# Optimization experiments

Measured on AMD Instinct MI355X. Metric: run time of the kernel, lower is better.

## Reference

```python
import jax, jax.numpy as jnp
import numpy as np

# Kernel offset table copied VERBATIM from the source (note the duplicated
# [-1,-1] row where [-1,1] would be expected -- we replicate the bug).
OFF = jnp.array([[-1, -1], [-1, 0], [-1, -1], [0, -1], [0, 0], [0, 1],
                 [1, -1], [1, 0], [1, 1]], dtype=jnp.float32)  # (9, 2)

T_HARD = 3.14 / 6
S_HARD = 2.0
S_RANGE = (S_HARD - 1.0 / S_HARD) / 2.0
H_VEC = jnp.array([T_HARD, S_RANGE, S_RANGE], dtype=jnp.float32)
B_VEC = jnp.array([0.0, S_RANGE, S_RANGE], dtype=jnp.float32)
BN_EPS = 1e-5


def setup_inputs() -> dict:
    key = jax.random.key(0)
    ks = jax.random.split(key, 9)
    N, C, H, W, O = 8, 128, 64, 64, 128
    return {
        "input_feat": jax.random.normal(ks[0], (N, C, H, W), jnp.float32),
        "ste_w": 0.05 * jax.random.normal(ks[1], (3, C, 1, 1), jnp.float32),
        "ste_b": 0.05 * jax.random.normal(ks[2], (3,), jnp.float32),
        "bn_gamma": 1.0 + 0.1 * jax.random.normal(ks[3], (3,), jnp.float32),
        "bn_beta": 0.1 * jax.random.normal(ks[4], (3,), jnp.float32),
        "bn_mean": 0.1 * jax.random.normal(ks[5], (3,), jnp.float32),
        "bn_var": jax.random.uniform(ks[6], (3,), jnp.float32, 0.5, 1.5),
        "dconv_w": jax.random.normal(ks[7], (O, C, 3, 3), jnp.float32) / np.sqrt(C * 9.0),
        "dconv_b": 0.05 * jax.random.normal(ks[8], (O,), jnp.float32),
    }


def _forward(input_feat, ste_w, ste_b, bn_gamma, bn_beta, bn_mean, bn_var,
             dconv_w, dconv_b):
    N, C, H, W = input_feat.shape
    O = dconv_w.shape[0]
    # --- ste: 1x1 conv -> BatchNorm (eval) -> tanh, then affine H*x + B ---
    s = jnp.einsum('nchw,oc->nohw', input_feat, ste_w[:, :, 0, 0])
    s = s + ste_b[None, :, None, None]
    scale = (bn_gamma / jnp.sqrt(bn_var + BN_EPS))
    s = (s - bn_mean[None, :, None, None]) * scale[None, :, None, None] \
        + bn_beta[None, :, None, None]
    info = jnp.tanh(s) * H_VEC[None, :, None, None] + B_VEC[None, :, None, None]
    # --- per-pixel 2x2 scaled rotation applied to kernel grid ---
    theta = info[:, 0]                  # [N,H,W]
    sin = jnp.sin(theta)
    cos = jnp.cos(theta)
    a00 = cos * info[:, 1]
    a11 = cos * info[:, 2]
    awt = jnp.stack([a00, -sin, sin, a11], axis=-1).reshape(N, H, W, 2, 2)
    offs = jnp.einsum('kd,nhwde->nkhwe', OFF, awt)   # [N,9,H,W,2]
    off_y = offs[..., 0]
    off_x = offs[..., 1]
    # --- deformable 3x3 conv, stride 1, padding 1, zero-pad bilinear ---
    k = jnp.arange(9)
    dy = (k // 3 - 1).astype(jnp.float32)  # default kernel y-offsets
    dx = (k % 3 - 1).astype(jnp.float32)
    yy = jnp.arange(H, dtype=jnp.float32)
    xx = jnp.arange(W, dtype=jnp.float32)
    y = yy[None, None, :, None] + dy[None, :, None, None] + off_y  # [N,9,H,W]
    x = xx[None, None, None, :] + dx[None, :, None, None] + off_x
    y0 = jnp.floor(y)
    x0 = jnp.floor(x)
    wy = y - y0
    wx = x - x0
    y0i = y0.astype(jnp.int32)
    x0i = x0.astype(jnp.int32)

    def gather(img, yi, xi):
        # img [C,H,W], yi/xi [9,H,W] -> [C,9,H,W], zero outside bounds
        valid = (yi >= 0) & (yi < H) & (xi >= 0) & (xi < W)
        v = img[:, jnp.clip(yi, 0, H - 1), jnp.clip(xi, 0, W - 1)]
        return v * valid[None].astype(img.dtype)

    def sample_one(img, y0i, x0i, wy, wx):
        v00 = gather(img, y0i, x0i)
        v01 = gather(img, y0i, x0i + 1)
        v10 = gather(img, y0i + 1, x0i)
        v11 = gather(img, y0i + 1, x0i + 1)
        return (v00 * ((1 - wy) * (1 - wx))[None]
                + v01 * ((1 - wy) * wx)[None]
                + v10 * (wy * (1 - wx))[None]
                + v11 * (wy * wx)[None])

    samp = jax.vmap(sample_one)(input_feat, y0i, x0i, wy, wx)  # [N,C,9,H,W]
    out = jnp.einsum('nckhw,ock->nohw', samp, dconv_w.reshape(O, C, 9))
    return out + dconv_b[None, :, None, None]


def reference(input_feat, ste_w, ste_b, bn_gamma, bn_beta, bn_mean, bn_var,
              dconv_w, dconv_b):
    return _forward(input_feat, ste_w, ste_b, bn_gamma, bn_beta, bn_mean,
                    bn_var, dconv_w, dconv_b)
```

## Files before the change

### kernel.cpp

```cpp
#include <hip/hip_runtime.h>

constexpr int kN = 8, kC = 128, kH = 64, kW = 64, kO = 128;
constexpr int kHW = kH * kW;

typedef float f32x4 __attribute__((ext_vector_type(4)));
typedef short bf16x8 __attribute__((ext_vector_type(8)));
typedef unsigned short ushort8 __attribute__((ext_vector_type(8)));

__device__ __forceinline__ float bf2f(unsigned short u) {
  unsigned int x = ((unsigned int)u) << 16;
  return __builtin_bit_cast(float, x);
}
__device__ __forceinline__ unsigned short f2bf(float f) {
  unsigned int b = __builtin_bit_cast(unsigned int, f);
  b += 0x7FFFu + ((b >> 16) & 1u);
  return (unsigned short)(b >> 16);
}

__global__ __launch_bounds__(256) void prep_kernel(
    const float* __restrict__ inp, const float* __restrict__ ste_w,
    const float* __restrict__ ste_b, const float* __restrict__ bn_g,
    const float* __restrict__ bn_b, const float* __restrict__ bn_m,
    const float* __restrict__ bn_v, unsigned short* __restrict__ nhwc,
    float* __restrict__ prm) {
  __shared__ float tile[kC * kW];
  __shared__ float part[4][3][kW];
  const int tid = threadIdx.x;
  const int nh = blockIdx.x;
  const int n = nh >> 6, h = nh & 63;
  const float* base = inp + (size_t)n * kC * kHW + h * kW;

  for (int i = tid; i < kC * kW; i += 256) {
    int c = i >> 6, w = i & 63;
    tile[i] = base[c * kHW + w];
  }
  __syncthreads();

  {
    const int w = tid & 63, cg = tid >> 6;
    float s0 = 0.f, s1 = 0.f, s2 = 0.f;
#pragma unroll 8
    for (int j = 0; j < 32; ++j) {
      int c = cg * 32 + j;
      float v = tile[c * kW + w];
      s0 += v * ste_w[c];
      s1 += v * ste_w[kC + c];
      s2 += v * ste_w[2 * kC + c];
    }
    part[cg][0][w] = s0;
    part[cg][1][w] = s1;
    part[cg][2][w] = s2;
  }
  __syncthreads();
  if (tid < kW) {
    const int w = tid;
    float s0 = part[0][0][w] + part[1][0][w] + part[2][0][w] + part[3][0][w];
    float s1 = part[0][1][w] + part[1][1][w] + part[2][1][w] + part[3][1][w];
    float s2 = part[0][2][w] + part[1][2][w] + part[2][2][w] + part[3][2][w];
    s0 = (s0 + ste_b[0] - bn_m[0]) * (bn_g[0] * rsqrtf(bn_v[0] + 1e-5f)) + bn_b[0];
    s1 = (s1 + ste_b[1] - bn_m[1]) * (bn_g[1] * rsqrtf(bn_v[1] + 1e-5f)) + bn_b[1];
    s2 = (s2 + ste_b[2] - bn_m[2]) * (bn_g[2] * rsqrtf(bn_v[2] + 1e-5f)) + bn_b[2];
    float th = tanhf(s0) * (3.14f / 6.0f);
    float i1 = tanhf(s1) * 0.75f + 0.75f;
    float i2 = tanhf(s2) * 0.75f + 0.75f;
    float sn = sinf(th), cs = cosf(th);
    prm[nh * 192 + w * 3 + 0] = cs * i1;
    prm[nh * 192 + w * 3 + 1] = sn;
    prm[nh * 192 + w * 3 + 2] = cs * i2;
  }

  for (int i = tid; i < kW * 16; i += 256) {
    int w = i & 63, ch = i >> 6;
    int c0 = ch * 8;
    ushort8 v;
#pragma unroll
    for (int j = 0; j < 8; ++j) v[j] = f2bf(tile[(c0 + j) * kW + w]);
    *(ushort8*)&nhwc[((size_t)(n * kH + h) * kW + w) * kC + c0] = v;
  }
}

__global__ __launch_bounds__(256) void reorder_bf16_kernel(
    const float* __restrict__ dw, unsigned short* __restrict__ wkb) {
  int idx = blockIdx.x * blockDim.x + threadIdx.x;
  if (idx >= 9 * kO * kC) return;
  int k = idx / (kO * kC);
  int r = idx - k * (kO * kC);
  int o = r >> 7, c = r & 127;
  wkb[idx] = f2bf(dw[(o * kC + c) * 9 + k]);
}

__global__ __launch_bounds__(512) void deform_mfma_kernel(
    const unsigned short* __restrict__ nhwc,
    const unsigned short* __restrict__ wkb,
    const float* __restrict__ prm, const float* __restrict__ db,
    float* __restrict__ out) {
  __shared__ __align__(16) unsigned short As[32 * 128];
  __shared__ __align__(16) unsigned short Bs[128 * 128];
  __shared__ float prmS[32 * 3];

  const int tid = threadIdx.x;
  const int lane = tid & 63, wave = tid >> 6;
  const int nh = blockIdx.x >> 1;
  const int w0 = (blockIdx.x & 1) << 5;
  const int n = nh >> 6, h = nh & 63;
  const unsigned short* nhwc_n = nhwc + (size_t)n * kH * kW * kC;

  if (tid < 96) prmS[tid] = prm[nh * 192 + w0 * 3 + tid];

  const int mg = wave >> 2, ng = wave & 3;
  const int row = mg * 16 + (lane & 15);
  const int kq = lane >> 4;
  const int rsw = (row & 7) << 4;
  f32x4 acc[2];
  acc[0] = (f32x4){0.f, 0.f, 0.f, 0.f};
  acc[1] = (f32x4){0.f, 0.f, 0.f, 0.f};

  for (int k = 0; k < 9; ++k) {
    __syncthreads();
    const float fdy = (float)(k / 3 - 1);
    const float fdx = (float)(k % 3 - 1);
    const float o0 = fdy;
    const float o1 = (k == 2) ? -1.0f : fdx;

    const unsigned short* wkp = wkb + (size_t)k * kO * kC;
#pragma unroll
    for (int it = 0; it < 4; ++it) {
      int i = tid + it * 512;
      int o = i >> 4, ch = i & 15;
      ushort8 v = *(const ushort8*)&wkp[o * kC + ch * 8];
      *(ushort8*)((char*)Bs + o * 256 + ((ch * 16) ^ ((o & 7) << 4))) = v;
    }

    {
      int p = tid >> 4, ch = tid & 15;
      float a00 = prmS[p * 3], sn = prmS[p * 3 + 1], a11 = prmS[p * 3 + 2];
      float y = (float)h + fdy + o0 * a00 + o1 * sn;
      float x = (float)(w0 + p) + fdx - o0 * sn + o1 * a11;
      float y0f = floorf(y), x0f = floorf(x);
      float wy = y - y0f, wx = x - x0f;
      int y0 = (int)y0f, x0 = (int)x0f;
      bool yv0 = (unsigned)y0 < (unsigned)kH;
      bool yv1 = (unsigned)(y0 + 1) < (unsigned)kH;
      bool xv0 = (unsigned)x0 < (unsigned)kW;
      bool xv1 = (unsigned)(x0 + 1) < (unsigned)kW;
      int y0c = min(max(y0, 0), kH - 1);
      int y1c = min(max(y0 + 1, 0), kH - 1);
      int x0c = min(max(x0, 0), kW - 1);
      int x1c = min(max(x0 + 1, 0), kW - 1);
      float w00 = (1.f - wy) * (1.f - wx) * (yv0 && xv0 ? 1.f : 0.f);
      float w01 = (1.f - wy) * wx * (yv0 && xv1 ? 1.f : 0.f);
      float w10 = wy * (1.f - wx) * (yv1 && xv0 ? 1.f : 0.f);
      float w11 = wy * wx * (yv1 && xv1 ? 1.f : 0.f);
      const int cb = ch * 8;
      ushort8 v00 = *(const ushort8*)&nhwc_n[((y0c * kW) + x0c) * kC + cb];
      ushort8 v01 = *(const ushort8*)&nhwc_n[((y0c * kW) + x1c) * kC + cb];
      ushort8 v10 = *(const ushort8*)&nhwc_n[((y1c * kW) + x0c) * kC + cb];
      ushort8 v11 = *(const ushort8*)&nhwc_n[((y1c * kW) + x1c) * kC + cb];
      ushort8 r;
#pragma unroll
      for (int j = 0; j < 8; ++j) {
        float val = bf2f(v00[j]) * w00 + bf2f(v01[j]) * w01 +
                    bf2f(v10[j]) * w10 + bf2f(v11[j]) * w11;
        r[j] = f2bf(val);
      }
      *(ushort8*)((char*)As + p * 256 + ((ch * 16) ^ ((p & 7) << 4))) = r;
    }
    __syncthreads();

#pragma unroll
    for (int ks = 0; ks < 4; ++ks) {
      const int kb = ks * 64 + kq * 16;
      bf16x8 a = *(const bf16x8*)((char*)As + row * 256 + (kb ^ rsw));
#pragma unroll
      for (int f = 0; f < 2; ++f) {
        const int orow = (ng * 2 + f) * 16 + (lane & 15);
        bf16x8 b = *(const bf16x8*)((char*)Bs + orow * 256 +
                                    (kb ^ ((orow & 7) << 4)));
        acc[f] = __builtin_amdgcn_mfma_f32_16x16x32_bf16(a, b, acc[f], 0, 0, 0);
      }
    }
  }

  const int pixb = mg * 16 + (lane >> 4) * 4;
#pragma unroll
  for (int f = 0; f < 2; ++f) {
    const int o = (ng * 2 + f) * 16 + (lane & 15);
    const float bias = db[o];
    float4 v = {acc[f][0] + bias, acc[f][1] + bias, acc[f][2] + bias,
                acc[f][3] + bias};
    *(float4*)&out[((size_t)(n * kO + o)) * kHW + h * kW + w0 + pixb] = v;
  }
}

__global__ __launch_bounds__(256) void deform_kernel_f32(
    const float* __restrict__ inp, const float* __restrict__ ste_w,
    const float* __restrict__ ste_b, const float* __restrict__ bn_g,
    const float* __restrict__ bn_b, const float* __restrict__ bn_m,
    const float* __restrict__ bn_v, const float* __restrict__ dw,
    const float* __restrict__ db, float* __restrict__ out) {
  __shared__ __align__(16) float smp[kC * 16];
  __shared__ float prm[16][3];
  const int tid = threadIdx.x;
  const int base = blockIdx.x * 16;
  const int n = base / kHW;
  const int hw = base - n * kHW;
  const int h = hw / kW;
  const int w0 = hw - h * kW;
  const float* inp_n = inp + (size_t)n * kC * kHW;

  for (int i = tid; i < kC * 16; i += 256) {
    int c = i >> 4, p = i & 15;
    smp[i] = inp_n[c * kHW + h * kW + w0 + p];
  }
  __syncthreads();
  {
    const int p = tid >> 4, cl = tid & 15;
    float a0 = 0.f, a1 = 0.f, a2 = 0.f;
#pragma unroll
    for (int i = 0; i < 8; ++i) {
      int c = cl + (i << 4);
      float v = smp[c * 16 + p];
      a0 += v * ste_w[c];
      a1 += v * ste_w[kC + c];
      a2 += v * ste_w[2 * kC + c];
    }
#pragma unroll
    for (int off = 8; off; off >>= 1) {
      a0 += __shfl_down(a0, off, 16);
      a1 += __shfl_down(a1, off, 16);
      a2 += __shfl_down(a2, off, 16);
    }
    if (cl == 0) {
      float s0 = (a0 + ste_b[0] - bn_m[0]) * (bn_g[0] * rsqrtf(bn_v[0] + 1e-5f)) + bn_b[0];
      float s1 = (a1 + ste_b[1] - bn_m[1]) * (bn_g[1] * rsqrtf(bn_v[1] + 1e-5f)) + bn_b[1];
      float s2 = (a2 + ste_b[2] - bn_m[2]) * (bn_g[2] * rsqrtf(bn_v[2] + 1e-5f)) + bn_b[2];
      float th = tanhf(s0) * (3.14f / 6.0f);
      float i1 = tanhf(s1) * 0.75f + 0.75f;
      float i2 = tanhf(s2) * 0.75f + 0.75f;
      prm[p][0] = cosf(th) * i1;
      prm[p][1] = sinf(th);
      prm[p][2] = cosf(th) * i2;
    }
  }
  const int o = tid & 127;
  const int ph = tid >> 7;
  float acc[8] = {0.f};
  for (int k = 0; k < 9; ++k) {
    __syncthreads();
    const float fdy = (float)(k / 3 - 1);
    const float fdx = (float)(k % 3 - 1);
    const float o0 = fdy;
    const float o1 = (k == 2) ? -1.0f : fdx;
    for (int i = tid; i < kC * 16; i += 256) {
      int c = i >> 4, p = i & 15;
      float a00 = prm[p][0], sn = prm[p][1], a11 = prm[p][2];
      float y = (float)h + fdy + o0 * a00 + o1 * sn;
      float x = (float)(w0 + p) + fdx - o0 * sn + o1 * a11;
      float y0f = floorf(y), x0f = floorf(x);
      float wy = y - y0f, wx = x - x0f;
      int y0 = (int)y0f, x0 = (int)x0f;
      const float* ic = inp_n + c * kHW;
      bool yv0 = (unsigned)y0 < (unsigned)kH;
      bool yv1 = (unsigned)(y0 + 1) < (unsigned)kH;
      bool xv0 = (unsigned)x0 < (unsigned)kW;
      bool xv1 = (unsigned)(x0 + 1) < (unsigned)kW;
      int y0c = min(max(y0, 0), kH - 1);
      int y1c = min(max(y0 + 1, 0), kH - 1);
      int x0c = min(max(x0, 0), kW - 1);
      int x1c = min(max(x0 + 1, 0), kW - 1);
      float v00 = (yv0 && xv0) ? ic[y0c * kW + x0c] : 0.f;
      float v01 = (yv0 && xv1) ? ic[y0c * kW + x1c] : 0.f;
      float v10 = (yv1 && xv0) ? ic[y1c * kW + x0c] : 0.f;
      float v11 = (yv1 && xv1) ? ic[y1c * kW + x1c] : 0.f;
      smp[i] = v00 * (1.f - wy) * (1.f - wx) + v01 * (1.f - wy) * wx +
               v10 * wy * (1.f - wx) + v11 * wy * wx;
    }
    __syncthreads();
    const float* wp = dw + (size_t)o * kC * 9 + k;
#pragma unroll 4
    for (int c = 0; c < kC; ++c) {
      float wv = wp[(size_t)c * 9];
      const float4 s0 = *(const float4*)&smp[c * 16 + (ph << 3)];
      const float4 s1 = *(const float4*)&smp[c * 16 + (ph << 3) + 4];
      acc[0] += wv * s0.x; acc[1] += wv * s0.y; acc[2] += wv * s0.z; acc[3] += wv * s0.w;
      acc[4] += wv * s1.x; acc[5] += wv * s1.y; acc[6] += wv * s1.z; acc[7] += wv * s1.w;
    }
  }
  const float bias = db[o];
  float* op = out + ((size_t)(n * kO + o)) * kHW + h * kW + w0 + (ph << 3);
#pragma unroll
  for (int j = 0; j < 8; ++j) op[j] = acc[j] + bias;
}

extern "C" void kernel_launch(void* const* d_in, const int* in_sizes, int n_in,
                              void* d_out, int out_size, void* d_ws, size_t ws_size,
                              hipStream_t stream) {
  const float* inp   = (const float*)d_in[0];
  const float* ste_w = (const float*)d_in[1];
  const float* ste_b = (const float*)d_in[2];
  const float* bn_g  = (const float*)d_in[3];
  const float* bn_b  = (const float*)d_in[4];
  const float* bn_m  = (const float*)d_in[5];
  const float* bn_v  = (const float*)d_in[6];
  const float* dw    = (const float*)d_in[7];
  const float* db    = (const float*)d_in[8];
  float* out = (float*)d_out;

  const size_t nhwc_bytes = (size_t)kN * kH * kW * kC * 2;
  const size_t wkb_bytes = (size_t)9 * kO * kC * 2;
  const size_t prm_bytes = (size_t)kN * kH * kW * 3 * 4;
  const size_t need = nhwc_bytes + wkb_bytes + prm_bytes;

  if (ws_size >= need) {
    unsigned short* nhwc = (unsigned short*)d_ws;
    unsigned short* wkb = (unsigned short*)((char*)d_ws + nhwc_bytes);
    float* prm = (float*)((char*)d_ws + nhwc_bytes + wkb_bytes);
    prep_kernel<<<kN * kH, 256, 0, stream>>>(inp, ste_w, ste_b, bn_g, bn_b,
                                             bn_m, bn_v, nhwc, prm);
    int wtot = 9 * kO * kC;
    reorder_bf16_kernel<<<(wtot + 255) / 256, 256, 0, stream>>>(dw, wkb);
    deform_mfma_kernel<<<kN * kH * 2, 512, 0, stream>>>(nhwc, wkb, prm, db, out);
  } else {
    deform_kernel_f32<<<kN * kHW / 16, 256, 0, stream>>>(
        inp, ste_w, ste_b, bn_g, bn_b, bn_m, bn_v, dw, db, out);
  }
}
```

Baseline: 53.79 us.

## Double-buffer LDS tiles and prefetch next tap's loads into registers

Each tap's weight tile and bilinear gather loads are now issued into registers before the current tap's MFMA loop, then written to the alternate LDS buffer afterward. This cuts one barrier per tap and hides global-load latency behind the matrix math. The per-pixel parameters are also loaded straight into registers instead of being staged through LDS. In exchange, LDS use roughly doubles to about 73 KB per block, which can reduce how many blocks fit per CU. The launch-bounds hint asking for 4 blocks may not be met and can raise register pressure.

```diff
diff --git a/kernel.cpp b/kernel.cpp
--- a/kernel.cpp
+++ b/kernel.cpp
@@ -89,14 +89,13 @@
   wkb[idx] = f2bf(dw[(o * kC + c) * 9 + k]);
 }
 
-__global__ __launch_bounds__(512) void deform_mfma_kernel(
+__global__ __launch_bounds__(512, 4) void deform_mfma_kernel(
     const unsigned short* __restrict__ nhwc,
     const unsigned short* __restrict__ wkb,
     const float* __restrict__ prm, const float* __restrict__ db,
     float* __restrict__ out) {
-  __shared__ __align__(16) unsigned short As[32 * 128];
-  __shared__ __align__(16) unsigned short Bs[128 * 128];
-  __shared__ float prmS[32 * 3];
+  __shared__ __align__(16) unsigned short As[2][32 * 128];
+  __shared__ __align__(16) unsigned short Bs[2][128 * 128];
 
   const int tid = threadIdx.x;
   const int lane = tid & 63, wave = tid >> 6;
@@ -105,7 +104,10 @@
   const int n = nh >> 6, h = nh & 63;
   const unsigned short* nhwc_n = nhwc + (size_t)n * kH * kW * kC;
 
-  if (tid < 96) prmS[tid] = prm[nh * 192 + w0 * 3 + tid];
+  const int p = tid >> 4, ch = tid & 15;
+  const float a00 = prm[nh * 192 + (w0 + p) * 3 + 0];
+  const float sn  = prm[nh * 192 + (w0 + p) * 3 + 1];
+  const float a11 = prm[nh * 192 + (w0 + p) * 3 + 2];
 
   const int mg = wave >> 2, ng = wave & 3;
   const int row = mg * 16 + (lane & 15);
@@ -115,70 +117,88 @@
   acc[0] = (f32x4){0.f, 0.f, 0.f, 0.f};
   acc[1] = (f32x4){0.f, 0.f, 0.f, 0.f};
 
-  for (int k = 0; k < 9; ++k) {
-    __syncthreads();
+  ushort8 bReg[4];
+  ushort8 a00r, a01r, a10r, a11r;
+  float w00, w01, w10, w11;
+
+  auto issue_tap = [&](int k) {
+    const unsigned short* wkp = wkb + (size_t)k * kO * kC;
+#pragma unroll
+    for (int it = 0; it < 4; ++it) {
+      int i = tid + it * 512;
+      int o = i >> 4, c8 = i & 15;
+      bReg[it] = *(const ushort8*)&wkp[o * kC + c8 * 8];
+    }
     const float fdy = (float)(k / 3 - 1);
     const float fdx = (float)(k % 3 - 1);
     const float o0 = fdy;
     const float o1 = (k == 2) ? -1.0f : fdx;
-
-    const unsigned short* wkp = wkb + (size_t)k * kO * kC;
+    float y = (float)h + fdy + o0 * a00 + o1 * sn;
+    float x = (float)(w0 + p) + fdx - o0 * sn + o1 * a11;
+    float y0f = floorf(y), x0f = floorf(x);
+    float wy = y - y0f, wx = x - x0f;
+    int y0 = (int)y0f, x0 = (int)x0f;
+    bool yv0 = (unsigned)y0 < (unsigned)kH;
+    bool yv1 = (unsigned)(y0 + 1) < (unsigned)kH;
+    bool xv0 = (unsigned)x0 < (unsigned)kW;
+    bool xv1 = (unsigned)(x0 + 1) < (unsigned)kW;
+    int y0c = min(max(y0, 0), kH - 1);
+    int y1c = min(max(y0 + 1, 0), kH - 1);
+    int x0c = min(max(x0, 0), kW - 1);
+    int x1c = min(max(x0 + 1, 0), kW - 1);
+    w00 = (1.f - wy) * (1.f - wx) * (yv0 && xv0 ? 1.f : 0.f);
+    w01 = (1.f - wy) * wx * (yv0 && xv1 ? 1.f : 0.f);
+    w10 = wy * (1.f - wx) * (yv1 && xv0 ? 1.f : 0.f);
+    w11 = wy * wx * (yv1 && xv1 ? 1.f : 0.f);
+    const int cb = ch * 8;
+    a00r = *(const ushort8*)&nhwc_n[((y0c * kW) + x0c) * kC + cb];
+    a01r = *(const ushort8*)&nhwc_n[((y0c * kW) + x1c) * kC + cb];
+    a10r = *(const ushort8*)&nhwc_n[((y1c * kW) + x0c) * kC + cb];
+    a11r = *(const ushort8*)&nhwc_n[((y1c * kW) + x1c) * kC + cb];
+  };
+
+  auto write_tiles = [&](int buf) {
 #pragma unroll
     for (int it = 0; it < 4; ++it) {
       int i = tid + it * 512;
-      int o = i >> 4, ch = i & 15;
-      ushort8 v = *(const ushort8*)&wkp[o * kC + ch * 8];
-      *(ushort8*)((char*)Bs + o * 256 + ((ch * 16) ^ ((o & 7) << 4))) = v;
-    }
-
-    {
-      int p = tid >> 4, ch = tid & 15;
-      float a00 = prmS[p * 3], sn = prmS[p * 3 + 1], a11 = prmS[p * 3 + 2];
-      float y = (float)h + fdy + o0 * a00 + o1 * sn;
-      float x = (float)(w0 + p) + fdx - o0 * sn + o1 * a11;
-      float y0f = floorf(y), x0f = floorf(x);
-      float wy = y - y0f, wx = x - x0f;
-      int y0 = (int)y0f, x0 = (int)x0f;
-      bool yv0 = (unsigned)y0 < (unsigned)kH;
-      bool yv1 = (unsigned)(y0 + 1) < (unsigned)kH;
-      bool xv0 = (unsigned)x0 < (unsigned)kW;
-      bool xv1 = (unsigned)(x0 + 1) < (unsigned)kW;
-      int y0c = min(max(y0, 0), kH - 1);
-      int y1c = min(max(y0 + 1, 0), kH - 1);
-      int x0c = min(max(x0, 0), kW - 1);
-      int x1c = min(max(x0 + 1, 0), kW - 1);
-      float w00 = (1.f - wy) * (1.f - wx) * (yv0 && xv0 ? 1.f : 0.f);
-      float w01 = (1.f - wy) * wx * (yv0 && xv1 ? 1.f : 0.f);
-      float w10 = wy * (1.f - wx) * (yv1 && xv0 ? 1.f : 0.f);
-      float w11 = wy * wx * (yv1 && xv1 ? 1.f : 0.f);
-      const int cb = ch * 8;
-      ushort8 v00 = *(const ushort8*)&nhwc_n[((y0c * kW) + x0c) * kC + cb];
-      ushort8 v01 = *(const ushort8*)&nhwc_n[((y0c * kW) + x1c) * kC + cb];
-      ushort8 v10 = *(const ushort8*)&nhwc_n[((y1c * kW) + x0c) * kC + cb];
-      ushort8 v11 = *(const ushort8*)&nhwc_n[((y1c * kW) + x1c) * kC + cb];
-      ushort8 r;
-#pragma unroll
-      for (int j = 0; j < 8; ++j) {
-        float val = bf2f(v00[j]) * w00 + bf2f(v01[j]) * w01 +
-                    bf2f(v10[j]) * w10 + bf2f(v11[j]) * w11;
-        r[j] = f2bf(val);
-      }
-      *(ushort8*)((char*)As + p * 256 + ((ch * 16) ^ ((p & 7) << 4))) = r;
-    }
-    __syncthreads();
-
+      int o = i >> 4, c8 = i & 15;
+      *(ushort8*)((char*)Bs[buf] + o * 256 + ((c8 * 16) ^ ((o & 7) << 4))) =
+          bReg[it];
+    }
+    ushort8 r;
+#pragma unroll
+    for (int j = 0; j < 8; ++j) {
+      float val = bf2f(a00r[j]) * w00 + bf2f(a01r[j]) * w01 +
+                  bf2f(a10r[j]) * w10 + bf2f(a11r[j]) * w11;
+      r[j] = f2bf(val);
+    }
+    *(ushort8*)((char*)As[buf] + p * 256 + ((ch * 16) ^ ((p & 7) << 4))) = r;
+  };
+
+  issue_tap(0);
+  write_tiles(0);
+  __syncthreads();
+
+  for (int k = 0; k < 9; ++k) {
+    const int cur = k & 1;
+    if (k < 8) issue_tap(k + 1);
+
+    const char* Ab = (const char*)As[cur];
+    const char* Bb = (const char*)Bs[cur];
 #pragma unroll
     for (int ks = 0; ks < 4; ++ks) {
       const int kb = ks * 64 + kq * 16;
-      bf16x8 a = *(const bf16x8*)((char*)As + row * 256 + (kb ^ rsw));
+      bf16x8 a = *(const bf16x8*)(Ab + row * 256 + (kb ^ rsw));
 #pragma unroll
       for (int f = 0; f < 2; ++f) {
         const int orow = (ng * 2 + f) * 16 + (lane & 15);
-        bf16x8 b = *(const bf16x8*)((char*)Bs + orow * 256 +
-                                    (kb ^ ((orow & 7) << 4)));
+        bf16x8 b = *(const bf16x8*)(Bb + orow * 256 + (kb ^ ((orow & 7) << 4)));
         acc[f] = __builtin_amdgcn_mfma_f32_16x16x32_bf16(a, b, acc[f], 0, 0, 0);
       }
     }
+
+    if (k < 8) write_tiles(cur ^ 1);
+    __syncthreads();
   }
 
   const int pixb = mg * 16 + (lane >> 4) * 4;
```

New measurement: 51.65 us. 4.0% less time.

## Gather all nine taps into LDS once and stream weights from global memory

Applied to the files above, without the earlier changes.

The weight-reorder kernel is folded into the prep kernel as extra blocks, which removes one launch. The MFMA kernel now samples all nine kernel taps into a single padded LDS A-tile, with a stride chosen to avoid bank conflicts, and needs only one barrier. Per-tap LDS staging of the B weights is dropped: B fragments are loaded straight from global memory, relying on L2/L1 caching. Loads of the bilinear-sampling parameters also go straight from global memory. This removes 18 barriers and the B-tile copy, but B reads now hit global memory inside the MFMA loop, and the A tile is larger, which may affect occupancy.

```diff
diff --git a/kernel.cpp b/kernel.cpp
--- a/kernel.cpp
+++ b/kernel.cpp
@@ -22,11 +22,24 @@
     const float* __restrict__ ste_b, const float* __restrict__ bn_g,
     const float* __restrict__ bn_b, const float* __restrict__ bn_m,
     const float* __restrict__ bn_v, unsigned short* __restrict__ nhwc,
-    float* __restrict__ prm) {
+    float* __restrict__ prm, const float* __restrict__ dw,
+    unsigned short* __restrict__ wkb) {
+  const int bid = blockIdx.x;
+  if (bid >= kN * kH) {
+    int idx = (bid - kN * kH) * 256 + threadIdx.x;
+    if (idx < 9 * kO * kC) {
+      int k = idx / (kO * kC);
+      int r = idx - k * (kO * kC);
+      int o = r >> 7, c = r & 127;
+      wkb[idx] = f2bf(dw[(o * kC + c) * 9 + k]);
+    }
+    return;
+  }
+
   __shared__ float tile[kC * kW];
   __shared__ float part[4][3][kW];
   const int tid = threadIdx.x;
-  const int nh = blockIdx.x;
+  const int nh = bid;
   const int n = nh >> 6, h = nh & 63;
   const float* base = inp + (size_t)n * kC * kHW + h * kW;
 
@@ -79,24 +92,14 @@
   }
 }
 
-__global__ __launch_bounds__(256) void reorder_bf16_kernel(
-    const float* __restrict__ dw, unsigned short* __restrict__ wkb) {
-  int idx = blockIdx.x * blockDim.x + threadIdx.x;
-  if (idx >= 9 * kO * kC) return;
-  int k = idx / (kO * kC);
-  int r = idx - k * (kO * kC);
-  int o = r >> 7, c = r & 127;
-  wkb[idx] = f2bf(dw[(o * kC + c) * 9 + k]);
-}
-
-__global__ __launch_bounds__(512) void deform_mfma_kernel(
+constexpr int kAStride = 1160;
+
+__global__ __launch_bounds__(512, 4) void deform_mfma_kernel(
     const unsigned short* __restrict__ nhwc,
     const unsigned short* __restrict__ wkb,
     const float* __restrict__ prm, const float* __restrict__ db,
     float* __restrict__ out) {
-  __shared__ __align__(16) unsigned short As[32 * 128];
-  __shared__ __align__(16) unsigned short Bs[128 * 128];
-  __shared__ float prmS[32 * 3];
+  __shared__ __align__(16) unsigned short As[32][kAStride];
 
   const int tid = threadIdx.x;
   const int lane = tid & 63, wave = tid >> 6;
@@ -105,79 +108,72 @@
   const int n = nh >> 6, h = nh & 63;
   const unsigned short* nhwc_n = nhwc + (size_t)n * kH * kW * kC;
 
-  if (tid < 96) prmS[tid] = prm[nh * 192 + w0 * 3 + tid];
-
-  const int mg = wave >> 2, ng = wave & 3;
-  const int row = mg * 16 + (lane & 15);
-  const int kq = lane >> 4;
-  const int rsw = (row & 7) << 4;
-  f32x4 acc[2];
-  acc[0] = (f32x4){0.f, 0.f, 0.f, 0.f};
-  acc[1] = (f32x4){0.f, 0.f, 0.f, 0.f};
-
+  const int p = tid >> 4, ch = tid & 15;
+  const float a00 = prm[nh * 192 + (w0 + p) * 3 + 0];
+  const float sn  = prm[nh * 192 + (w0 + p) * 3 + 1];
+  const float a11 = prm[nh * 192 + (w0 + p) * 3 + 2];
+  const int cb = ch * 8;
+
+#pragma unroll
   for (int k = 0; k < 9; ++k) {
-    __syncthreads();
     const float fdy = (float)(k / 3 - 1);
     const float fdx = (float)(k % 3 - 1);
     const float o0 = fdy;
     const float o1 = (k == 2) ? -1.0f : fdx;
-
-    const unsigned short* wkp = wkb + (size_t)k * kO * kC;
-#pragma unroll
-    for (int it = 0; it < 4; ++it) {
-      int i = tid + it * 512;
-      int o = i >> 4, ch = i & 15;
-      ushort8 v = *(const ushort8*)&wkp[o * kC + ch * 8];
-      *(ushort8*)((char*)Bs + o * 256 + ((ch * 16) ^ ((o & 7) << 4))) = v;
-    }
-
-    {
-      int p = tid >> 4, ch = tid & 15;
-      float a00 = prmS[p * 3], sn = prmS[p * 3 + 1], a11 = prmS[p * 3 + 2];
-      float y = (float)h + fdy + o0 * a00 + o1 * sn;
-      float x = (float)(w0 + p) + fdx - o0 * sn + o1 * a11;
-      float y0f = floorf(y), x0f = floorf(x);
-      float wy = y - y0f, wx = x - x0f;
-      int y0 = (int)y0f, x0 = (int)x0f;
-      bool yv0 = (unsigned)y0 < (unsigned)kH;
-      bool yv1 = (unsigned)(y0 + 1) < (unsigned)kH;
-      bool xv0 = (unsigned)x0 < (unsigned)kW;
-      bool xv1 = (unsigned)(x0 + 1) < (unsigned)kW;
-      int y0c = min(max(y0, 0), kH - 1);
-      int y1c = min(max(y0 + 1, 0), kH - 1);
-      int x0c = min(max(x0, 0), kW - 1);
-      int x1c = min(max(x0 + 1, 0), kW - 1);
-      float w00 = (1.f - wy) * (1.f - wx) * (yv0 && xv0 ? 1.f : 0.f);
-      float w01 = (1.f - wy) * wx * (yv0 && xv1 ? 1.f : 0.f);
-      float w10 = wy * (1.f - wx) * (yv1 && xv0 ? 1.f : 0.f);
-      float w11 = wy * wx * (yv1 && xv1 ? 1.f : 0.f);
-      const int cb = ch * 8;
-      ushort8 v00 = *(const ushort8*)&nhwc_n[((y0c * kW) + x0c) * kC + cb];
-      ushort8 v01 = *(const ushort8*)&nhwc_n[((y0c * kW) + x1c) * kC + cb];
-      ushort8 v10 = *(const ushort8*)&nhwc_n[((y1c * kW) + x0c) * kC + cb];
-      ushort8 v11 = *(const ushort8*)&nhwc_n[((y1c * kW) + x1c) * kC + cb];
-      ushort8 r;
-#pragma unroll
-      for (int j = 0; j < 8; ++j) {
-        float val = bf2f(v00[j]) * w00 + bf2f(v01[j]) * w01 +
-                    bf2f(v10[j]) * w10 + bf2f(v11[j]) * w11;
-        r[j] = f2bf(val);
-      }
-      *(ushort8*)((char*)As + p * 256 + ((ch * 16) ^ ((p & 7) << 4))) = r;
-    }
-    __syncthreads();
-
+    float y = (float)h + fdy + o0 * a00 + o1 * sn;
+    float x = (float)(w0 + p) + fdx - o0 * sn + o1 * a11;
+    float y0f = floorf(y), x0f = floorf(x);
+    float wy = y - y0f, wx = x - x0f;
+    int y0 = (int)y0f, x0 = (int)x0f;
+    bool yv0 = (unsigned)y0 < (unsigned)kH;
+    bool yv1 = (unsigned)(y0 + 1) < (unsigned)kH;
+    bool xv0 = (unsigned)x0 < (unsigned)kW;
+    bool xv1 = (unsigned)(x0 + 1) < (unsigned)kW;
+    int y0c = min(max(y0, 0), kH - 1);
+    int y1c = min(max(y0 + 1, 0), kH - 1);
+    int x0c = min(max(x0, 0), kW - 1);
+    int x1c = min(max(x0 + 1, 0), kW - 1);
+    float w00 = (1.f - wy) * (1.f - wx) * (yv0 && xv0 ? 1.f : 0.f);
+    float w01 = (1.f - wy) * wx * (yv0 && xv1 ? 1.f : 0.f);
+    float w10 = wy * (1.f - wx) * (yv1 && xv0 ? 1.f : 0.f);
+    float w11 = wy * wx * (yv1 && xv1 ? 1.f : 0.f);
+    ushort8 v00 = *(const ushort8*)&nhwc_n[((y0c * kW) + x0c) * kC + cb];
+    ushort8 v01 = *(const ushort8*)&nhwc_n[((y0c * kW) + x1c) * kC + cb];
+    ushort8 v10 = *(const ushort8*)&nhwc_n[((y1c * kW) + x0c) * kC + cb];
+    ushort8 v11 = *(const ushort8*)&nhwc_n[((y1c * kW) + x1c) * kC + cb];
+    ushort8 r;
+#pragma unroll
+    for (int j = 0; j < 8; ++j) {
+      float val = bf2f(v00[j]) * w00 + bf2f(v01[j]) * w01 +
+                  bf2f(v10[j]) * w10 + bf2f(v11[j]) * w11;
+      r[j] = f2bf(val);
+    }
+    *(ushort8*)&As[p][k * 128 + ch * 8] = r;
+  }
+  __syncthreads();
+
+  const int mg = wave >> 2, ng = wave & 3;
+  const int row = mg * 16 + (lane & 15);
+  const int kq = lane >> 4;
+  const char* Arow = (const char*)&As[row][0];
+  f32x4 acc[2];
+  acc[0] = (f32x4){0.f, 0.f, 0.f, 0.f};
+  acc[1] = (f32x4){0.f, 0.f, 0.f, 0.f};
+
+  const int oc0 = (ng * 2) * 16 + (lane & 15);
+  const int oc1 = (ng * 2 + 1) * 16 + (lane & 15);
+  const char* B0 = (const char*)wkb + oc0 * 256 + kq * 16;
+  const char* B1 = (const char*)wkb + oc1 * 256 + kq * 16;
+
+#pragma unroll
+  for (int k = 0; k < 9; ++k) {
 #pragma unroll
     for (int ks = 0; ks < 4; ++ks) {
-      const int kb = ks * 64 + kq * 16;
-      bf16x8 a = *(const bf16x8*)((char*)As + row * 256 + (kb ^ rsw));
-#pragma unroll
-      for (int f = 0; f < 2; ++f) {
-        const int orow = (ng * 2 + f) * 16 + (lane & 15);
-        bf16x8 b = *(const bf16x8*)((char*)Bs + orow * 256 +
-                                    (kb ^ ((orow & 7) << 4)));
-        acc[f] = __builtin_amdgcn_mfma_f32_16x16x32_bf16(a, b, acc[f], 0, 0, 0);
-      }
+      bf16x8 a = *(const bf16x8*)(Arow + k * 256 + ks * 64 + kq * 16);
+      bf16x8 b0 = *(const bf16x8*)(B0 + k * 32768 + ks * 64);
+      bf16x8 b1 = *(const bf16x8*)(B1 + k * 32768 + ks * 64);
+      acc[0] = __builtin_amdgcn_mfma_f32_16x16x32_bf16(a, b0, acc[0], 0, 0, 0);
+      acc[1] = __builtin_amdgcn_mfma_f32_16x16x32_bf16(a, b1, acc[1], 0, 0, 0);
     }
   }
 
@@ -315,10 +311,9 @@
     unsigned short* nhwc = (unsigned short*)d_ws;
     unsigned short* wkb = (unsigned short*)((char*)d_ws + nhwc_bytes);
     float* prm = (float*)((char*)d_ws + nhwc_bytes + wkb_bytes);
-    prep_kernel<<<kN * kH, 256, 0, stream>>>(inp, ste_w, ste_b, bn_g, bn_b,
-                                             bn_m, bn_v, nhwc, prm);
-    int wtot = 9 * kO * kC;
-    reorder_bf16_kernel<<<(wtot + 255) / 256, 256, 0, stream>>>(dw, wkb);
+    const int reorder_blocks = (9 * kO * kC + 255) / 256;
+    prep_kernel<<<kN * kH + reorder_blocks, 256, 0, stream>>>(
+        inp, ste_w, ste_b, bn_g, bn_b, bn_m, bn_v, nhwc, prm, dw, wkb);
     deform_mfma_kernel<<<kN * kH * 2, 512, 0, stream>>>(nhwc, wkb, prm, db, out);
   } else {
     deform_kernel_f32<<<kN * kHW / 16, 256, 0, stream>>>(
```

Result: slower. 96.12 us (+78.7%).
